# Optimization experiments

Hardware: AMD Instinct MI355X
Metric: run time of the kernel (lower is better)

Reference implementation:

```python
import jax, jax.numpy as jnp
import numpy as np

D_MODEL = 1024
D_KEY = 64
N_HEADS = 16
B, T = 4, 2048


def setup_inputs() -> dict:
    key = jax.random.key(0)
    ks = jax.random.split(key, 12)
    s = 0.02
    return {
        "keys": jax.random.normal(ks[0], (B, T, D_MODEL), jnp.float32),
        "queries": jax.random.normal(ks[1], (B, T, D_MODEL), jnp.float32),
        "values": jax.random.normal(ks[2], (B, T, D_MODEL), jnp.float32),
        "pad_mask": jnp.ones((B, T), jnp.int32),
        "WK_w": jax.random.normal(ks[3], (D_KEY * N_HEADS, D_MODEL), jnp.float32) * s,
        "WK_b": jnp.zeros((D_KEY * N_HEADS,), jnp.float32),
        "WQ_w": jax.random.normal(ks[4], (D_KEY * N_HEADS, D_MODEL), jnp.float32) * s,
        "WQ_b": jnp.zeros((D_KEY * N_HEADS,), jnp.float32),
        "WV_w": jax.random.normal(ks[5], (D_KEY * N_HEADS, D_MODEL), jnp.float32) * s,
        "WV_b": jnp.zeros((D_KEY * N_HEADS,), jnp.float32),
        "WO_w": jax.random.normal(ks[6], (D_MODEL, D_KEY * N_HEADS), jnp.float32) * s,
        "WO_b": jnp.zeros((D_MODEL,), jnp.float32),
    }


def reference(keys, queries, values, pad_mask, WK_w, WK_b, WQ_w, WQ_b, WV_w, WV_b, WO_w, WO_b):
    # NOTE: the original torch module calls masked_fill (non-inplace) and discards
    # the result, so neither the causal mask nor pad_mask has any effect. We
    # faithfully reproduce that: no masking. pad_mask is an unused constant.
    batch, time = keys.shape[:2]
    k = keys @ WK_w.T + WK_b      # [B,T,H*dk]
    q = queries @ WQ_w.T + WQ_b
    v = values @ WV_w.T + WV_b

    def split_heads(x):
        return x.reshape(batch, time, N_HEADS, D_KEY).transpose(0, 2, 1, 3)  # [B,H,T,dk]

    k, q, v = split_heads(k), split_heads(q), split_heads(v)
    # scores[t,s] = k_t . q_s / sqrt(d_key)  (K and Q swapped, as in source)
    scores = jnp.einsum("bhtd,bhsd->bhts", k, q) / jnp.sqrt(jnp.float32(D_KEY))
    attn = jax.nn.softmax(scores, axis=-1)             # [B,H,T,T]
    ctx = jnp.einsum("bhts,bhsd->bhtd", attn, v)       # [B,H,T,dk]
    ctx = ctx.transpose(0, 2, 1, 3).reshape(batch, time, N_HEADS * D_KEY)
    return ctx @ WO_w.T + WO_b
```

## Files before the change

kernel.cpp:

```cpp
#include <hip/hip_runtime.h>

typedef unsigned short u16;
typedef unsigned int u32;
typedef __attribute__((ext_vector_type(8))) short short8;
typedef __attribute__((ext_vector_type(4))) float f32x4;

__device__ __forceinline__ u16 f2bf(float f) {
    unsigned int u = __float_as_uint(f);
    u += 0x7fffu + ((u >> 16) & 1u);
    return (u16)(u >> 16);
}

__device__ __forceinline__ u32 pack_trunc(float a, float b) {
    return __builtin_amdgcn_perm(__float_as_uint(b), __float_as_uint(a), 0x07060302u);
}

__device__ __forceinline__ void gload16(const u16* g, const u16* l) {
    __builtin_amdgcn_global_load_lds(
        (const __attribute__((address_space(1))) unsigned int*)g,
        (__attribute__((address_space(3))) unsigned int*)l, 16, 0, 0);
}

__global__ __launch_bounds__(256) void cast_all(const float* __restrict__ k,
                                                const float* __restrict__ q,
                                                const float* __restrict__ v,
                                                const float* __restrict__ wk,
                                                const float* __restrict__ wq,
                                                const float* __restrict__ wv,
                                                const float* __restrict__ wo,
                                                u16* __restrict__ Xk, u16* __restrict__ Xq,
                                                u16* __restrict__ Xv, u16* __restrict__ Wk,
                                                u16* __restrict__ Wq, u16* __restrict__ Wv,
                                                u16* __restrict__ Wo) {
    size_t i = ((size_t)blockIdx.x * 256 + threadIdx.x) * 8;
    const float* src; u16* dst; size_t off;
    if (i < 25165824) {
        int r = (int)(i >> 23); off = i & 8388607;
        src = r == 0 ? k : (r == 1 ? q : v);
        dst = r == 0 ? Xk : (r == 1 ? Xq : Xv);
    } else {
        size_t j = i - 25165824;
        int r = (int)(j >> 20); off = j & 1048575;
        src = r == 0 ? wk : (r == 1 ? wq : (r == 2 ? wv : wo));
        dst = r == 0 ? Wk : (r == 1 ? Wq : (r == 2 ? Wv : Wo));
    }
    float4 a = *(const float4*)(src + off);
    float4 b = *(const float4*)(src + off + 4);
    union { u16 h[8]; uint4 u; } r8;
    r8.h[0] = f2bf(a.x); r8.h[1] = f2bf(a.y); r8.h[2] = f2bf(a.z); r8.h[3] = f2bf(a.w);
    r8.h[4] = f2bf(b.x); r8.h[5] = f2bf(b.y); r8.h[6] = f2bf(b.z); r8.h[7] = f2bf(b.w);
    *(uint4*)(dst + off) = r8.u;
}

__global__ __launch_bounds__(256) void gemm128(const u16* __restrict__ X,
                                               const u16* __restrict__ W,
                                               const float* __restrict__ bias,
                                               float* __restrict__ outF,
                                               u16* __restrict__ outB,
                                               int mode, float scale) {
    __shared__ u16 sA[128 * 32];
    __shared__ u16 sB[128 * 32];
    const int tid  = threadIdx.x;
    const int wave = tid >> 6, lane = tid & 63;
    const int quad = lane >> 4, l16 = lane & 15;
    const int wm = wave & 1, wn = wave >> 1;
    const int i0 = blockIdx.y * 128, j0 = blockIdx.x * 128;
    const int lrow = tid >> 2, lseg = tid & 3;

    f32x4 acc[4][4];
    #pragma unroll
    for (int mt = 0; mt < 4; mt++)
        #pragma unroll
        for (int nt = 0; nt < 4; nt++) acc[mt][nt] = (f32x4){0.f, 0.f, 0.f, 0.f};

    const u16* gA0 = X + (size_t)(i0 + lrow) * 1024 + lseg * 8;
    const u16* gA1 = X + (size_t)(i0 + 64 + lrow) * 1024 + lseg * 8;
    const u16* gB0 = W + (size_t)(j0 + lrow) * 1024 + lseg * 8;
    const u16* gB1 = W + (size_t)(j0 + 64 + lrow) * 1024 + lseg * 8;
    const u16* lA0 = sA + wave * 512;
    const u16* lA1 = sA + 2048 + wave * 512;
    const u16* lB0 = sB + wave * 512;
    const u16* lB1 = sB + 2048 + wave * 512;

    for (int kk = 0; kk < 1024; kk += 32) {
        __syncthreads();
        gload16(gA0 + kk, lA0);
        gload16(gA1 + kk, lA1);
        gload16(gB0 + kk, lB0);
        gload16(gB1 + kk, lB1);
        __syncthreads();
        short8 af[4], bf[4];
        #pragma unroll
        for (int mt = 0; mt < 4; mt++)
            af[mt] = *(const short8*)&sA[(wm * 64 + mt * 16 + l16) * 32 + quad * 8];
        #pragma unroll
        for (int nt = 0; nt < 4; nt++)
            bf[nt] = *(const short8*)&sB[(wn * 64 + nt * 16 + l16) * 32 + quad * 8];
        #pragma unroll
        for (int mt = 0; mt < 4; mt++)
            #pragma unroll
            for (int nt = 0; nt < 4; nt++)
                acc[mt][nt] = __builtin_amdgcn_mfma_f32_16x16x32_bf16(af[mt], bf[nt], acc[mt][nt], 0, 0, 0);
    }

    #pragma unroll
    for (int mt = 0; mt < 4; mt++) {
        #pragma unroll
        for (int nt = 0; nt < 4; nt++) {
            int j = j0 + wn * 64 + nt * 16 + l16;
            float bj = bias[j];
            #pragma unroll
            for (int r = 0; r < 4; r++) {
                int i = i0 + wm * 64 + mt * 16 + quad * 4 + r;
                float v = (acc[mt][nt][r] + bj) * scale;
                if (mode == 1) {
                    outF[(size_t)i * 1024 + j] = v;
                } else {
                    int b = i >> 11, t = i & 2047;
                    int h = j >> 6,  dd = j & 63;
                    size_t idx;
                    if (mode == 0) idx = (((size_t)(b * 16 + h)) * 2048 + t) * 64 + dd;
                    else           idx = (((size_t)(b * 16 + h)) * 64 + dd) * 2048 + t;
                    outB[idx] = f2bf(v);
                }
            }
        }
    }
}

#define QST 72

__global__ __launch_bounds__(256, 4) void attn_kernel(const u16* __restrict__ Kbh,
                                                      const u16* __restrict__ Qbh,
                                                      const u16* __restrict__ Vtg,
                                                      u16* __restrict__ ctx) {
    __shared__ u16 sQ[64 * QST];
    __shared__ u16 sVt[64 * QST];
    __shared__ u16 sP[8 * 16 * QST];
    const int tid  = threadIdx.x;
    const int wave = tid >> 6, lane = tid & 63;
    const int quad = lane >> 4, l16 = lane & 15;
    const int bh = blockIdx.y;
    const int t0 = blockIdx.x * 128;
    const int tw = t0 + wave * 32;
    const size_t base = (size_t)bh * 2048 * 64;

    short8 bk[2][2];
    #pragma unroll
    for (int g = 0; g < 2; g++) {
        const u16* kr = Kbh + base + (size_t)(tw + g * 16 + l16) * 64 + quad * 8;
        bk[g][0] = *(const short8*)kr;
        bk[g][1] = *(const short8*)(kr + 32);
    }
    const short8 ones = {0x3F80, 0x3F80, 0x3F80, 0x3F80, 0x3F80, 0x3F80, 0x3F80, 0x3F80};

    f32x4 accO[2][4];
    #pragma unroll
    for (int g = 0; g < 2; g++)
        #pragma unroll
        for (int dt = 0; dt < 4; dt++) accO[g][dt] = (f32x4){0.f, 0.f, 0.f, 0.f};
    f32x4 accL[2];
    accL[0] = (f32x4){0.f, 0.f, 0.f, 0.f};
    accL[1] = (f32x4){0.f, 0.f, 0.f, 0.f};

    const int srow = tid >> 2, seg = tid & 3;
    u16* sPw = sP + wave * 2 * 16 * QST;

    for (int s0 = 0; s0 < 2048; s0 += 64) {
        __syncthreads();
        {
            const uint4* gq = (const uint4*)(Qbh + base + (size_t)(s0 + srow) * 64 + seg * 16);
            uint4 q0 = gq[0], q1 = gq[1];
            *(uint4*)&sQ[srow * QST + seg * 16]     = q0;
            *(uint4*)&sQ[srow * QST + seg * 16 + 8] = q1;
        }
        {
            const uint4* gv = (const uint4*)(Vtg + ((size_t)bh * 64 + srow) * 2048 + s0 + seg * 16);
            uint4 v0 = gv[0], v1 = gv[1];
            *(uint4*)&sVt[srow * QST + seg * 16]     = v0;
            *(uint4*)&sVt[srow * QST + seg * 16 + 8] = v1;
        }
        __syncthreads();

        f32x4 accS[2][4];
        #pragma unroll
        for (int nt = 0; nt < 4; nt++) {
            short8 aq0 = *(const short8*)&sQ[(nt * 16 + l16) * QST + quad * 8];
            short8 aq1 = *(const short8*)&sQ[(nt * 16 + l16) * QST + 32 + quad * 8];
            #pragma unroll
            for (int g = 0; g < 2; g++) {
                f32x4 s = __builtin_amdgcn_mfma_f32_16x16x32_bf16(aq0, bk[g][0],
                            (f32x4){0.f, 0.f, 0.f, 0.f}, 0, 0, 0);
                accS[g][nt] = __builtin_amdgcn_mfma_f32_16x16x32_bf16(aq1, bk[g][1], s, 0, 0, 0);
            }
        }

        #pragma unroll
        for (int g = 0; g < 2; g++) {
            u16* row = sPw + (g * 16 + l16) * QST;
            #pragma unroll
            for (int nt = 0; nt < 4; nt++) {
                float p0 = exp2f(accS[g][nt][0]);
                float p1 = exp2f(accS[g][nt][1]);
                float p2 = exp2f(accS[g][nt][2]);
                float p3 = exp2f(accS[g][nt][3]);
                uint2 pk = { pack_trunc(p0, p1), pack_trunc(p2, p3) };
                *(uint2*)&row[nt * 16 + quad * 4] = pk;
            }
        }

        #pragma unroll
        for (int kk = 0; kk < 2; kk++) {
            short8 av[4];
            #pragma unroll
            for (int dt = 0; dt < 4; dt++)
                av[dt] = *(const short8*)&sVt[(dt * 16 + l16) * QST + kk * 32 + quad * 8];
            #pragma unroll
            for (int g = 0; g < 2; g++) {
                short8 bp = *(const short8*)&sPw[(g * 16 + l16) * QST + kk * 32 + quad * 8];
                accL[g] = __builtin_amdgcn_mfma_f32_16x16x32_bf16(ones, bp, accL[g], 0, 0, 0);
                #pragma unroll
                for (int dt = 0; dt < 4; dt++)
                    accO[g][dt] = __builtin_amdgcn_mfma_f32_16x16x32_bf16(av[dt], bp, accO[g][dt], 0, 0, 0);
            }
        }
    }

    const int b = bh >> 4, h = bh & 15;
    #pragma unroll
    for (int g = 0; g < 2; g++) {
        float inv = 1.f / accL[g][0];
        int t = tw + g * 16 + l16;
        u16* orow = ctx + ((size_t)(b * 2048 + t)) * 1024 + h * 64;
        #pragma unroll
        for (int dt = 0; dt < 4; dt++) {
            union { u16 h4[4]; uint2 u; } o;
            #pragma unroll
            for (int r = 0; r < 4; r++) o.h4[r] = f2bf(accO[g][dt][r] * inv);
            *(uint2*)&orow[dt * 16 + quad * 4] = o.u;
        }
    }
}

extern "C" void kernel_launch(void* const* d_in, const int* in_sizes, int n_in,
                              void* d_out, int out_size, void* d_ws, size_t ws_size,
                              hipStream_t stream) {
    const float* keys    = (const float*)d_in[0];
    const float* queries = (const float*)d_in[1];
    const float* values  = (const float*)d_in[2];
    const float* WKb = (const float*)d_in[5];
    const float* WQb = (const float*)d_in[7];
    const float* WVb = (const float*)d_in[9];
    const float* WOb = (const float*)d_in[11];

    char* ws = (char*)d_ws;
    const size_t MB = 1 << 20;
    u16* Kbh = (u16*)(ws + 0 * MB);
    u16* Qbh = (u16*)(ws + 16 * MB);
    u16* Vtg = (u16*)(ws + 32 * MB);
    u16* Xk  = (u16*)(ws + 48 * MB);
    u16* Xq  = (u16*)(ws + 64 * MB);
    u16* Xv  = (u16*)(ws + 80 * MB);
    u16* Wk  = (u16*)(ws + 96 * MB);
    u16* Wq  = (u16*)(ws + 98 * MB);
    u16* Wv  = (u16*)(ws + 100 * MB);
    u16* Wo  = (u16*)(ws + 102 * MB);
    u16* ctx = (u16*)(ws + 48 * MB);

    cast_all<<<14336, 256, 0, stream>>>(keys, queries, values,
                                        (const float*)d_in[4], (const float*)d_in[6],
                                        (const float*)d_in[8], (const float*)d_in[10],
                                        Xk, Xq, Xv, Wk, Wq, Wv, Wo);

    const float kscale = 1.4426950408889634f * 0.125f;
    dim3 gg(8, 64);
    gemm128<<<gg, 256, 0, stream>>>(Xk, Wk, WKb, nullptr, Kbh, 0, kscale);
    gemm128<<<gg, 256, 0, stream>>>(Xq, Wq, WQb, nullptr, Qbh, 0, 1.0f);
    gemm128<<<gg, 256, 0, stream>>>(Xv, Wv, WVb, nullptr, Vtg, 2, 1.0f);

    attn_kernel<<<dim3(16, 64), 256, 0, stream>>>(Kbh, Qbh, Vtg, ctx);

    gemm128<<<gg, 256, 0, stream>>>(ctx, Wo, WOb, (float*)d_out, nullptr, 1, 1.0f);
}
```

Before: 401.4 us.

## Batch QKV GEMMs, enlarge attention tile per wave, narrow output GEMM tile

The three QKV projection GEMMs become one launch using blockIdx.z, which removes launch gaps and gives a larger grid. The attention kernel now handles 64 query rows per wave instead of 32, so each Q/V tile load from shared memory is reused across more rows. It interleaves S, exp and PV per 16-row group with a double-buffered P scratch and uses the native exp2 builtin, at the cost of more registers and lower occupancy. The output projection uses 128x64 tiles to double its block count and improve CU coverage.

After: 364.5 us. -9.2%, faster.

```diff
diff --git a/kernel.cpp b/kernel.cpp
--- a/kernel.cpp
+++ b/kernel.cpp
@@ -52,14 +52,28 @@
     *(uint4*)(dst + off) = r8.u;
 }
 
-__global__ __launch_bounds__(256) void gemm128(const u16* __restrict__ X,
-                                               const u16* __restrict__ W,
-                                               const float* __restrict__ bias,
-                                               float* __restrict__ outF,
-                                               u16* __restrict__ outB,
-                                               int mode, float scale) {
+__global__ __launch_bounds__(256) void gemm_qkv(const u16* __restrict__ Xk,
+                                                const u16* __restrict__ Xq,
+                                                const u16* __restrict__ Xv,
+                                                const u16* __restrict__ Wk,
+                                                const u16* __restrict__ Wq,
+                                                const u16* __restrict__ Wv,
+                                                const float* __restrict__ bK,
+                                                const float* __restrict__ bQ,
+                                                const float* __restrict__ bV,
+                                                u16* __restrict__ Kbh,
+                                                u16* __restrict__ Qbh,
+                                                u16* __restrict__ Vtg,
+                                                float kscale) {
     __shared__ u16 sA[128 * 32];
     __shared__ u16 sB[128 * 32];
+    const int z = blockIdx.z;
+    const u16* X = z == 0 ? Xk : (z == 1 ? Xq : Xv);
+    const u16* W = z == 0 ? Wk : (z == 1 ? Wq : Wv);
+    const float* bias = z == 0 ? bK : (z == 1 ? bQ : bV);
+    u16* out = z == 0 ? Kbh : (z == 1 ? Qbh : Vtg);
+    const float scale = z == 0 ? kscale : 1.0f;
+
     const int tid  = threadIdx.x;
     const int wave = tid >> 6, lane = tid & 63;
     const int quad = lane >> 4, l16 = lane & 15;
@@ -113,16 +127,74 @@
             for (int r = 0; r < 4; r++) {
                 int i = i0 + wm * 64 + mt * 16 + quad * 4 + r;
                 float v = (acc[mt][nt][r] + bj) * scale;
-                if (mode == 1) {
-                    outF[(size_t)i * 1024 + j] = v;
-                } else {
-                    int b = i >> 11, t = i & 2047;
-                    int h = j >> 6,  dd = j & 63;
-                    size_t idx;
-                    if (mode == 0) idx = (((size_t)(b * 16 + h)) * 2048 + t) * 64 + dd;
-                    else           idx = (((size_t)(b * 16 + h)) * 64 + dd) * 2048 + t;
-                    outB[idx] = f2bf(v);
-                }
+                int b = i >> 11, t = i & 2047;
+                int h = j >> 6,  dd = j & 63;
+                size_t idx;
+                if (z == 2) idx = (((size_t)(b * 16 + h)) * 64 + dd) * 2048 + t;
+                else        idx = (((size_t)(b * 16 + h)) * 2048 + t) * 64 + dd;
+                out[idx] = f2bf(v);
+            }
+        }
+    }
+}
+
+__global__ __launch_bounds__(256) void gemm_out(const u16* __restrict__ X,
+                                                const u16* __restrict__ W,
+                                                const float* __restrict__ bias,
+                                                float* __restrict__ out) {
+    __shared__ u16 sA[128 * 32];
+    __shared__ u16 sB[64 * 32];
+    const int tid  = threadIdx.x;
+    const int wave = tid >> 6, lane = tid & 63;
+    const int quad = lane >> 4, l16 = lane & 15;
+    const int wm = wave & 1, wn = wave >> 1;
+    const int i0 = blockIdx.y * 128, j0 = blockIdx.x * 64;
+    const int lrow = tid >> 2, lseg = tid & 3;
+
+    f32x4 acc[4][2];
+    #pragma unroll
+    for (int mt = 0; mt < 4; mt++) {
+        acc[mt][0] = (f32x4){0.f, 0.f, 0.f, 0.f};
+        acc[mt][1] = (f32x4){0.f, 0.f, 0.f, 0.f};
+    }
+
+    const u16* gA0 = X + (size_t)(i0 + lrow) * 1024 + lseg * 8;
+    const u16* gA1 = X + (size_t)(i0 + 64 + lrow) * 1024 + lseg * 8;
+    const u16* gB0 = W + (size_t)(j0 + lrow) * 1024 + lseg * 8;
+    const u16* lA0 = sA + wave * 512;
+    const u16* lA1 = sA + 2048 + wave * 512;
+    const u16* lB0 = sB + wave * 512;
+
+    for (int kk = 0; kk < 1024; kk += 32) {
+        __syncthreads();
+        gload16(gA0 + kk, lA0);
+        gload16(gA1 + kk, lA1);
+        gload16(gB0 + kk, lB0);
+        __syncthreads();
+        short8 af[4], bf[2];
+        #pragma unroll
+        for (int mt = 0; mt < 4; mt++)
+            af[mt] = *(const short8*)&sA[(wm * 64 + mt * 16 + l16) * 32 + quad * 8];
+        #pragma unroll
+        for (int nt = 0; nt < 2; nt++)
+            bf[nt] = *(const short8*)&sB[(wn * 32 + nt * 16 + l16) * 32 + quad * 8];
+        #pragma unroll
+        for (int mt = 0; mt < 4; mt++)
+            #pragma unroll
+            for (int nt = 0; nt < 2; nt++)
+                acc[mt][nt] = __builtin_amdgcn_mfma_f32_16x16x32_bf16(af[mt], bf[nt], acc[mt][nt], 0, 0, 0);
+    }
+
+    #pragma unroll
+    for (int mt = 0; mt < 4; mt++) {
+        #pragma unroll
+        for (int nt = 0; nt < 2; nt++) {
+            int j = j0 + wn * 32 + nt * 16 + l16;
+            float bj = bias[j];
+            #pragma unroll
+            for (int r = 0; r < 4; r++) {
+                int i = i0 + wm * 64 + mt * 16 + quad * 4 + r;
+                out[(size_t)i * 1024 + j] = acc[mt][nt][r] + bj;
             }
         }
     }
@@ -130,38 +202,38 @@
 
 #define QST 72
 
-__global__ __launch_bounds__(256, 4) void attn_kernel(const u16* __restrict__ Kbh,
+__global__ __launch_bounds__(256, 2) void attn_kernel(const u16* __restrict__ Kbh,
                                                       const u16* __restrict__ Qbh,
                                                       const u16* __restrict__ Vtg,
                                                       u16* __restrict__ ctx) {
     __shared__ u16 sQ[64 * QST];
     __shared__ u16 sVt[64 * QST];
-    __shared__ u16 sP[8 * 16 * QST];
+    __shared__ u16 sP[4 * 2 * 16 * QST];
     const int tid  = threadIdx.x;
     const int wave = tid >> 6, lane = tid & 63;
     const int quad = lane >> 4, l16 = lane & 15;
     const int bh = blockIdx.y;
-    const int t0 = blockIdx.x * 128;
-    const int tw = t0 + wave * 32;
+    const int t0 = blockIdx.x * 256;
+    const int tw = t0 + wave * 64;
     const size_t base = (size_t)bh * 2048 * 64;
 
-    short8 bk[2][2];
-    #pragma unroll
-    for (int g = 0; g < 2; g++) {
+    short8 bk[4][2];
+    #pragma unroll
+    for (int g = 0; g < 4; g++) {
         const u16* kr = Kbh + base + (size_t)(tw + g * 16 + l16) * 64 + quad * 8;
         bk[g][0] = *(const short8*)kr;
         bk[g][1] = *(const short8*)(kr + 32);
     }
     const short8 ones = {0x3F80, 0x3F80, 0x3F80, 0x3F80, 0x3F80, 0x3F80, 0x3F80, 0x3F80};
 
-    f32x4 accO[2][4];
-    #pragma unroll
-    for (int g = 0; g < 2; g++)
+    f32x4 accO[4][4];
+    #pragma unroll
+    for (int g = 0; g < 4; g++)
         #pragma unroll
         for (int dt = 0; dt < 4; dt++) accO[g][dt] = (f32x4){0.f, 0.f, 0.f, 0.f};
-    f32x4 accL[2];
-    accL[0] = (f32x4){0.f, 0.f, 0.f, 0.f};
-    accL[1] = (f32x4){0.f, 0.f, 0.f, 0.f};
+    f32x4 accL[4];
+    #pragma unroll
+    for (int g = 0; g < 4; g++) accL[g] = (f32x4){0.f, 0.f, 0.f, 0.f};
 
     const int srow = tid >> 2, seg = tid & 3;
     u16* sPw = sP + wave * 2 * 16 * QST;
@@ -182,53 +254,51 @@
         }
         __syncthreads();
 
-        f32x4 accS[2][4];
+        short8 aq[4][2], av[2][4];
         #pragma unroll
         for (int nt = 0; nt < 4; nt++) {
-            short8 aq0 = *(const short8*)&sQ[(nt * 16 + l16) * QST + quad * 8];
-            short8 aq1 = *(const short8*)&sQ[(nt * 16 + l16) * QST + 32 + quad * 8];
-            #pragma unroll
-            for (int g = 0; g < 2; g++) {
-                f32x4 s = __builtin_amdgcn_mfma_f32_16x16x32_bf16(aq0, bk[g][0],
+            aq[nt][0] = *(const short8*)&sQ[(nt * 16 + l16) * QST + quad * 8];
+            aq[nt][1] = *(const short8*)&sQ[(nt * 16 + l16) * QST + 32 + quad * 8];
+        }
+        #pragma unroll
+        for (int kk = 0; kk < 2; kk++)
+            #pragma unroll
+            for (int dt = 0; dt < 4; dt++)
+                av[kk][dt] = *(const short8*)&sVt[(dt * 16 + l16) * QST + kk * 32 + quad * 8];
+
+        #pragma unroll
+        for (int g = 0; g < 4; g++) {
+            f32x4 aS[4];
+            #pragma unroll
+            for (int nt = 0; nt < 4; nt++) {
+                f32x4 s = __builtin_amdgcn_mfma_f32_16x16x32_bf16(aq[nt][0], bk[g][0],
                             (f32x4){0.f, 0.f, 0.f, 0.f}, 0, 0, 0);
-                accS[g][nt] = __builtin_amdgcn_mfma_f32_16x16x32_bf16(aq1, bk[g][1], s, 0, 0, 0);
-            }
-        }
-
-        #pragma unroll
-        for (int g = 0; g < 2; g++) {
-            u16* row = sPw + (g * 16 + l16) * QST;
+                aS[nt] = __builtin_amdgcn_mfma_f32_16x16x32_bf16(aq[nt][1], bk[g][1], s, 0, 0, 0);
+            }
+            u16* pb = sPw + (g & 1) * 16 * QST;
             #pragma unroll
             for (int nt = 0; nt < 4; nt++) {
-                float p0 = exp2f(accS[g][nt][0]);
-                float p1 = exp2f(accS[g][nt][1]);
-                float p2 = exp2f(accS[g][nt][2]);
-                float p3 = exp2f(accS[g][nt][3]);
+                float p0 = __builtin_amdgcn_exp2f(aS[nt][0]);
+                float p1 = __builtin_amdgcn_exp2f(aS[nt][1]);
+                float p2 = __builtin_amdgcn_exp2f(aS[nt][2]);
+                float p3 = __builtin_amdgcn_exp2f(aS[nt][3]);
                 uint2 pk = { pack_trunc(p0, p1), pack_trunc(p2, p3) };
-                *(uint2*)&row[nt * 16 + quad * 4] = pk;
-            }
-        }
-
-        #pragma unroll
-        for (int kk = 0; kk < 2; kk++) {
-            short8 av[4];
-            #pragma unroll
-            for (int dt = 0; dt < 4; dt++)
-                av[dt] = *(const short8*)&sVt[(dt * 16 + l16) * QST + kk * 32 + quad * 8];
-            #pragma unroll
-            for (int g = 0; g < 2; g++) {
-                short8 bp = *(const short8*)&sPw[(g * 16 + l16) * QST + kk * 32 + quad * 8];
+                *(uint2*)&pb[l16 * QST + nt * 16 + quad * 4] = pk;
+            }
+            #pragma unroll
+            for (int kk = 0; kk < 2; kk++) {
+                short8 bp = *(const short8*)&pb[l16 * QST + kk * 32 + quad * 8];
                 accL[g] = __builtin_amdgcn_mfma_f32_16x16x32_bf16(ones, bp, accL[g], 0, 0, 0);
                 #pragma unroll
                 for (int dt = 0; dt < 4; dt++)
-                    accO[g][dt] = __builtin_amdgcn_mfma_f32_16x16x32_bf16(av[dt], bp, accO[g][dt], 0, 0, 0);
+                    accO[g][dt] = __builtin_amdgcn_mfma_f32_16x16x32_bf16(av[kk][dt], bp, accO[g][dt], 0, 0, 0);
             }
         }
     }
 
     const int b = bh >> 4, h = bh & 15;
     #pragma unroll
-    for (int g = 0; g < 2; g++) {
+    for (int g = 0; g < 4; g++) {
         float inv = 1.f / accL[g][0];
         int t = tw + g * 16 + l16;
         u16* orow = ctx + ((size_t)(b * 2048 + t)) * 1024 + h * 64;
@@ -273,12 +343,10 @@
                                         Xk, Xq, Xv, Wk, Wq, Wv, Wo);
 
     const float kscale = 1.4426950408889634f * 0.125f;
-    dim3 gg(8, 64);
-    gemm128<<<gg, 256, 0, stream>>>(Xk, Wk, WKb, nullptr, Kbh, 0, kscale);
-    gemm128<<<gg, 256, 0, stream>>>(Xq, Wq, WQb, nullptr, Qbh, 0, 1.0f);
-    gemm128<<<gg, 256, 0, stream>>>(Xv, Wv, WVb, nullptr, Vtg, 2, 1.0f);
-
-    attn_kernel<<<dim3(16, 64), 256, 0, stream>>>(Kbh, Qbh, Vtg, ctx);
-
-    gemm128<<<gg, 256, 0, stream>>>(ctx, Wo, WOb, (float*)d_out, nullptr, 1, 1.0f);
-}
+    gemm_qkv<<<dim3(8, 64, 3), 256, 0, stream>>>(Xk, Xq, Xv, Wk, Wq, Wv,
+                                                 WKb, WQb, WVb, Kbh, Qbh, Vtg, kscale);
+
+    attn_kernel<<<dim3(8, 64), 256, 0, stream>>>(Kbh, Qbh, Vtg, ctx);
+
+    gemm_out<<<dim3(16, 64), 256, 0, stream>>>(ctx, Wo, WOb, (float*)d_out);
+}
```
